# Kernel optimization log

Hardware: AMD Instinct MI355X
Metric: run time of the kernel (lower is better)

Reference implementation:

```python
import jax, jax.numpy as jnp
import numpy as np

B, S, T = 4, 1024, 2048
HID = 1024
NH = 16
NKV = 4
HD = HID // NH  # 64


def setup_inputs() -> dict:
    key = jax.random.key(0)
    ks = jax.random.split(key, 6)
    scale = 1.0 / np.sqrt(HID)
    return {
        "x": jax.random.normal(ks[0], (B, S, HID), dtype=jnp.float32),
        "context": jax.random.normal(ks[1], (B, T, HID), dtype=jnp.float32),
        "Wq": jax.random.normal(ks[2], (NH * HD, HID), dtype=jnp.float32) * scale,
        "Wk": jax.random.normal(ks[3], (NKV * HD, HID), dtype=jnp.float32) * scale,
        "Wv": jax.random.normal(ks[4], (NKV * HD, HID), dtype=jnp.float32) * scale,
        "Wo": jax.random.normal(ks[5], (HID, NH * HD), dtype=jnp.float32) * scale,
    }


def reference(x, context, Wq, Wk, Wv, Wo):
    Bx, Sx, _ = x.shape
    Tx = context.shape[1]
    rep = NH // NKV
    # projections (Linear with no bias: y = x @ W.T)
    q = (x @ Wq.T).reshape(Bx, Sx, NKV, rep, HD)          # group query heads by KV head
    k = (context @ Wk.T).reshape(Bx, Tx, NKV, HD)
    v = (context @ Wv.T).reshape(Bx, Tx, NKV, HD)
    scale = 1.0 / jnp.sqrt(jnp.asarray(HD, dtype=q.dtype))
    # scores: [B, NKV, rep, S, T] -- shares K across the rep grouped heads
    # (math-identical to repeat_interleave then SDPA, without materializing K/V copies)
    scores = jnp.einsum("bsgrd,btgd->bgrst", q, k) * scale
    attn = jax.nn.softmax(scores, axis=-1)
    out = jnp.einsum("bgrst,btgd->bsgrd", attn, v)        # [B,S,NKV,rep,HD]
    out = out.reshape(Bx, Sx, NH * HD)
    return out @ Wo.T
```

## Files before the change

### kernel.cpp

```cpp
#include <hip/hip_runtime.h>
#include <hip/hip_bf16.h>
#include <stdint.h>

typedef __bf16 bf16x8 __attribute__((ext_vector_type(8)));
typedef float f32x4 __attribute__((ext_vector_type(4)));
typedef unsigned short u16;
typedef unsigned int u32;

struct __align__(8) us4 { u16 x, y, z, w; };
struct __align__(16) us8 { u16 v[8]; };

#define LOG2E 1.44269504088896f
#define QSCALE (0.125f * LOG2E)

__device__ __forceinline__ void async_load16(const void* g, void* l) {
    __builtin_amdgcn_global_load_lds(
        (const __attribute__((address_space(1))) u32*)(uintptr_t)g,
        (__attribute__((address_space(3))) u32*)(u32)(uintptr_t)l,
        16, 0, 0);
}

__device__ __forceinline__ u16 f2bfbits(float f) {
    __bf16 h = (__bf16)f;
    return __builtin_bit_cast(u16, h);
}

__global__ __launch_bounds__(256) void convert_all(
    const float* __restrict__ x, const float* __restrict__ ctx,
    const float* __restrict__ wq, const float* __restrict__ wk,
    const float* __restrict__ wv, const float* __restrict__ wo,
    u16* __restrict__ xb, u16* __restrict__ ctxb, u16* __restrict__ wqb,
    u16* __restrict__ wkb, u16* __restrict__ wvb, u16* __restrict__ wob) {
    int i = blockIdx.x * 256 + threadIdx.x;
    const float* s; u16* d; int j;
    if (i < 524288)        { s = x;   d = xb;   j = i; }
    else if (i < 1572864)  { s = ctx; d = ctxb; j = i - 524288; }
    else if (i < 1703936)  { s = wq;  d = wqb;  j = i - 1572864; }
    else if (i < 1736704)  { s = wk;  d = wkb;  j = i - 1703936; }
    else if (i < 1769472)  { s = wv;  d = wvb;  j = i - 1736704; }
    else                   { s = wo;  d = wob;  j = i - 1769472; }
    const float4* sp = (const float4*)s + (size_t)j * 2;
    float4 a = sp[0], b = sp[1];
    us8 o;
    o.v[0] = f2bfbits(a.x); o.v[1] = f2bfbits(a.y);
    o.v[2] = f2bfbits(a.z); o.v[3] = f2bfbits(a.w);
    o.v[4] = f2bfbits(b.x); o.v[5] = f2bfbits(b.y);
    o.v[6] = f2bfbits(b.z); o.v[7] = f2bfbits(b.w);
    *(us8*)(d + (size_t)j * 8) = o;
}

__global__ __launch_bounds__(256) void proj_qkv(
    const u16* __restrict__ xb, const u16* __restrict__ ctxb,
    const u16* __restrict__ Wqb, const u16* __restrict__ Wkb,
    const u16* __restrict__ Wvb,
    u16* __restrict__ q, u16* __restrict__ k2, u16* __restrict__ vT) {
    __shared__ u16 As[128 * 64];
    __shared__ u16 Bs[128 * 64];
    const int tid = threadIdx.x;
    const int w = tid >> 6, lane = tid & 63, quad = lane >> 4, id = lane & 15;
    const int wr = (w >> 1) * 64, wc = (w & 1) * 64;
    const int lrow = lane >> 3, lcol = (lane & 7) * 8;

    const int bid = blockIdx.x;
    const u16 *A, *Bm;
    int mtile, ntile, mode;
    if (bid < 256) {
        mode = 0; A = xb; Bm = Wqb;
        mtile = (bid >> 3) * 128; ntile = (bid & 7) * 128;
    } else if (bid < 384) {
        int s2 = bid - 256;
        mode = 1; A = ctxb; Bm = Wkb;
        mtile = (s2 >> 1) * 128; ntile = (s2 & 1) * 128;
    } else {
        int s2 = bid - 384;
        mode = 2; A = ctxb; Bm = Wvb;
        mtile = (s2 >> 1) * 128; ntile = (s2 & 1) * 128;
    }

    f32x4 acc[4][4];
#pragma unroll
    for (int i = 0; i < 4; i++)
#pragma unroll
        for (int j = 0; j < 4; j++) acc[i][j] = (f32x4){0.f, 0.f, 0.f, 0.f};

    for (int k0 = 0; k0 < 1024; k0 += 64) {
        __syncthreads();
#pragma unroll
        for (int is = 0; is < 4; is++) {
            int r = is * 32 + w * 8 + lrow;
            async_load16(A + (size_t)(mtile + r) * 1024 + k0 + lcol, &As[(is * 32 + w * 8) * 64]);
        }
#pragma unroll
        for (int is = 0; is < 4; is++) {
            int r = is * 32 + w * 8 + lrow;
            async_load16(Bm + (size_t)(ntile + r) * 1024 + k0 + lcol, &Bs[(is * 32 + w * 8) * 64]);
        }
        __syncthreads();
#pragma unroll
        for (int kk = 0; kk < 2; kk++) {
            bf16x8 af[4], bfr[4];
#pragma unroll
            for (int i = 0; i < 4; i++)
                af[i] = *(const bf16x8*)&As[(wr + i * 16 + id) * 64 + kk * 32 + quad * 8];
#pragma unroll
            for (int j = 0; j < 4; j++)
                bfr[j] = *(const bf16x8*)&Bs[(wc + j * 16 + id) * 64 + kk * 32 + quad * 8];
#pragma unroll
            for (int i = 0; i < 4; i++)
#pragma unroll
                for (int j = 0; j < 4; j++)
                    acc[i][j] = __builtin_amdgcn_mfma_f32_16x16x32_bf16(af[i], bfr[j], acc[i][j], 0, 0, 0);
        }
    }

#pragma unroll
    for (int i = 0; i < 4; i++)
#pragma unroll
        for (int j = 0; j < 4; j++) {
            int mbase = mtile + wr + i * 16 + quad * 4;
            int n = ntile + wc + j * 16 + id;
            if (mode == 2) {
                int b = mbase >> 11, t = mbase & 2047;
                int g = n >> 6, d = n & 63;
                us4 pk;
                pk.x = f2bfbits(acc[i][j][0]);
                pk.y = f2bfbits(acc[i][j][1]);
                pk.z = f2bfbits(acc[i][j][2]);
                pk.w = f2bfbits(acc[i][j][3]);
                *(us4*)&vT[((size_t)((b << 2) + g) * 64 + d) * 2048 + t] = pk;
            } else if (mode == 1) {
#pragma unroll
                for (int r = 0; r < 4; r++) {
                    int m = mbase + r;
                    int b = m >> 11, t = m & 2047;
                    int g = n >> 6, d = n & 63;
                    k2[((size_t)((b << 2) + g) * 2048 + t) * 64 + d] = f2bfbits(acc[i][j][r]);
                }
            } else {
#pragma unroll
                for (int r = 0; r < 4; r++)
                    q[(size_t)(mbase + r) * 1024 + n] = f2bfbits(acc[i][j][r] * QSCALE);
            }
        }
}

__global__ __launch_bounds__(256) void gemm_out(const u16* __restrict__ A,
                                                const u16* __restrict__ Bm,
                                                float* __restrict__ C) {
    __shared__ u16 As[128 * 64];
    __shared__ u16 Bs[128 * 64];
    const int tid = threadIdx.x;
    const int w = tid >> 6, lane = tid & 63, quad = lane >> 4, id = lane & 15;
    const int mtile = blockIdx.y * 128, ntile = blockIdx.x * 128;
    const int wr = (w >> 1) * 64, wc = (w & 1) * 64;
    const int lrow = lane >> 3, lcol = (lane & 7) * 8;

    f32x4 acc[4][4];
#pragma unroll
    for (int i = 0; i < 4; i++)
#pragma unroll
        for (int j = 0; j < 4; j++) acc[i][j] = (f32x4){0.f, 0.f, 0.f, 0.f};

    for (int k0 = 0; k0 < 1024; k0 += 64) {
        __syncthreads();
#pragma unroll
        for (int is = 0; is < 4; is++) {
            int r = is * 32 + w * 8 + lrow;
            async_load16(A + (size_t)(mtile + r) * 1024 + k0 + lcol, &As[(is * 32 + w * 8) * 64]);
        }
#pragma unroll
        for (int is = 0; is < 4; is++) {
            int r = is * 32 + w * 8 + lrow;
            async_load16(Bm + (size_t)(ntile + r) * 1024 + k0 + lcol, &Bs[(is * 32 + w * 8) * 64]);
        }
        __syncthreads();
#pragma unroll
        for (int kk = 0; kk < 2; kk++) {
            bf16x8 af[4], bfr[4];
#pragma unroll
            for (int i = 0; i < 4; i++)
                af[i] = *(const bf16x8*)&As[(wr + i * 16 + id) * 64 + kk * 32 + quad * 8];
#pragma unroll
            for (int j = 0; j < 4; j++)
                bfr[j] = *(const bf16x8*)&Bs[(wc + j * 16 + id) * 64 + kk * 32 + quad * 8];
#pragma unroll
            for (int i = 0; i < 4; i++)
#pragma unroll
                for (int j = 0; j < 4; j++)
                    acc[i][j] = __builtin_amdgcn_mfma_f32_16x16x32_bf16(af[i], bfr[j], acc[i][j], 0, 0, 0);
        }
    }

#pragma unroll
    for (int i = 0; i < 4; i++)
#pragma unroll
        for (int j = 0; j < 4; j++) {
            int mbase = mtile + wr + i * 16 + quad * 4;
            int n = ntile + wc + j * 16 + id;
#pragma unroll
            for (int r = 0; r < 4; r++)
                C[(size_t)(mbase + r) * 1024 + n] = acc[i][j][r];
        }
}

__global__ __launch_bounds__(256, 2) void attn_kernel(const u16* __restrict__ q,
                                                      const u16* __restrict__ k2,
                                                      const u16* __restrict__ vT,
                                                      u16* __restrict__ o) {
    __shared__ u16 Ks[2][64 * 64];
    __shared__ u16 Vt[2][64 * 64];
    const int tid = threadIdx.x;
    const int w = tid >> 6, lane = tid & 63, quad = lane >> 4, id = lane & 15;

    const int bid = blockIdx.x;
    const int xcd = bid & 7, slot = bid >> 3;
    const int bg = xcd * 2 + (slot >> 5);
    const int inner = slot & 31;
    const int b = bg >> 2, g = bg & 3;
    const int h = g * 4 + (inner >> 3);
    const int s0 = (inner & 7) * 128;

    const int stgswz = (((lane & 7) ^ (lane >> 3) ^ ((w & 1) << 2))) * 8;
    int kfkey[2];
#pragma unroll
    for (int c = 0; c < 2; c++)
        kfkey[c] = (id & 3) | (((c ^ ((id >> 2) & 1)) & 1) << 2);
    const int vkey = (id & 7) ^ (((id >> 3) & 1) << 2);
    const int trow_base = ((id & 12) << 1) + (id & 3);

    bf16x8 qf[2][2];
#pragma unroll
    for (int rb = 0; rb < 2; rb++) {
        const size_t base = ((size_t)(b * 1024 + s0 + w * 32 + rb * 16 + id)) * 1024 + h * 64;
        qf[rb][0] = *(const bf16x8*)&q[base + quad * 8];
        qf[rb][1] = *(const bf16x8*)&q[base + 32 + quad * 8];
    }

    bf16x8 ones;
    {
        __bf16 one = (__bf16)1.0f;
#pragma unroll
        for (int i = 0; i < 8; i++) ones[i] = one;
    }

    f32x4 acc[2][4], accl[2];
#pragma unroll
    for (int rb = 0; rb < 2; rb++) {
        accl[rb] = (f32x4){0.f, 0.f, 0.f, 0.f};
#pragma unroll
        for (int i = 0; i < 4; i++) acc[rb][i] = (f32x4){0.f, 0.f, 0.f, 0.f};
    }

    const size_t kbase = ((size_t)(b * 4 + g)) * 2048 * 64;
    const size_t vbase = ((size_t)(b * 4 + g)) * 64 * 2048;

    auto stage = [&](int t0, int buf) {
#pragma unroll
        for (int is = 0; is < 2; is++) {
            int tl = is * 32 + w * 8;
            async_load16(&k2[kbase + (size_t)(t0 + tl + (lane >> 3)) * 64 + stgswz],
                         &Ks[buf][tl * 64]);
        }
#pragma unroll
        for (int is = 0; is < 2; is++) {
            int dl = is * 32 + w * 8;
            async_load16(&vT[vbase + (size_t)(dl + (lane >> 3)) * 2048 + t0 + stgswz],
                         &Vt[buf][dl * 64]);
        }
    };

    stage(0, 0);
    __syncthreads();

    int cur = 0;
    for (int t0 = 0; t0 < 2048; t0 += 64) {
        if (t0 + 64 < 2048) stage(t0 + 64, cur ^ 1);

        f32x4 s[2][2][2];
#pragma unroll
        for (int kk = 0; kk < 2; kk++)
#pragma unroll
            for (int P = 0; P < 2; P++)
#pragma unroll
                for (int c = 0; c < 2; c++) {
                    int trow = P * 32 + trow_base + c * 4;
                    bf16x8 kf = *(const bf16x8*)&Ks[cur][trow * 64 + (((kk * 4 + quad) ^ kfkey[c]) * 8)];
#pragma unroll
                    for (int rb = 0; rb < 2; rb++)
                        s[rb][P][c] = __builtin_amdgcn_mfma_f32_16x16x32_bf16(
                            kf, qf[rb][kk],
                            kk ? s[rb][P][c] : (f32x4){0.f, 0.f, 0.f, 0.f}, 0, 0, 0);
                }

        bf16x8 pa[2][2];
#pragma unroll
        for (int rb = 0; rb < 2; rb++)
#pragma unroll
            for (int P = 0; P < 2; P++) {
                bf16x8 t;
#pragma unroll
                for (int c = 0; c < 2; c++)
#pragma unroll
                    for (int r = 0; r < 4; r++)
                        t[c * 4 + r] = (__bf16)__builtin_exp2f(s[rb][P][c][r]);
                pa[rb][P] = t;
            }

#pragma unroll
        for (int P = 0; P < 2; P++) {
#pragma unroll
            for (int db = 0; db < 4; db++) {
                bf16x8 vf = *(const bf16x8*)&Vt[cur][(db * 16 + id) * 64 + (((P * 4 + quad) ^ vkey) * 8)];
#pragma unroll
                for (int rb = 0; rb < 2; rb++)
                    acc[rb][db] = __builtin_amdgcn_mfma_f32_16x16x32_bf16(pa[rb][P], vf, acc[rb][db], 0, 0, 0);
            }
#pragma unroll
            for (int rb = 0; rb < 2; rb++)
                accl[rb] = __builtin_amdgcn_mfma_f32_16x16x32_bf16(pa[rb][P], ones, accl[rb], 0, 0, 0);
        }

        __syncthreads();
        cur ^= 1;
    }

#pragma unroll
    for (int rb = 0; rb < 2; rb++) {
        f32x4 inv;
#pragma unroll
        for (int r = 0; r < 4; r++) inv[r] = 1.0f / accl[rb][r];
#pragma unroll
        for (int db = 0; db < 4; db++)
#pragma unroll
            for (int r = 0; r < 4; r++) {
                int srow = s0 + w * 32 + rb * 16 + quad * 4 + r;
                o[((size_t)(b * 1024 + srow)) * 1024 + h * 64 + db * 16 + id] =
                    f2bfbits(acc[rb][db][r] * inv[r]);
            }
    }
}

extern "C" void kernel_launch(void* const* d_in, const int* in_sizes, int n_in,
                              void* d_out, int out_size, void* d_ws, size_t ws_size,
                              hipStream_t stream) {
    (void)in_sizes; (void)n_in; (void)out_size; (void)ws_size;
    const float* x   = (const float*)d_in[0];
    const float* ctx = (const float*)d_in[1];
    const float* Wq  = (const float*)d_in[2];
    const float* Wk  = (const float*)d_in[3];
    const float* Wv  = (const float*)d_in[4];
    const float* Wo  = (const float*)d_in[5];
    float* out = (float*)d_out;

    u16* xb   = (u16*)d_ws;
    u16* ctxb = xb   + 4096 * 1024;
    u16* Wqb  = ctxb + 4 * 2048 * 1024;
    u16* Wkb  = Wqb  + 1024 * 1024;
    u16* Wvb  = Wkb  + 256 * 1024;
    u16* Wob  = Wvb  + 256 * 1024;
    u16* q    = Wob  + 1024 * 1024;
    u16* k2   = q    + 4096 * 1024;
    u16* vT   = k2   + 4 * 4 * 2048 * 64;
    u16* o    = vT   + 4 * 4 * 64 * 2048;

    convert_all<<<7424, 256, 0, stream>>>(x, ctx, Wq, Wk, Wv, Wo,
                                          xb, ctxb, Wqb, Wkb, Wvb, Wob);
    proj_qkv<<<512, 256, 0, stream>>>(xb, ctxb, Wqb, Wkb, Wvb, q, k2, vT);
    attn_kernel<<<512, 256, 0, stream>>>(q, k2, vT, o);
    gemm_out<<<dim3(8, 32), 256, 0, stream>>>(o, Wob, out);
}
```

Before: 210.4 us.

## Fuse fp32-to-bf16 conversion into GEMM loads and use fp16 for PV

Removes the separate conversion kernel. The projection and output GEMMs now stage fp32 tiles into LDS with an XOR swizzle and convert them to bf16 when building fragments. This saves one pass over the inputs and one launch, but doubles LDS use and global-to-LDS traffic per tile in the GEMMs. Separately, V and the softmax probabilities switch to fp16 with packed RTZ conversion and fp16 MFMA for the PV product, which cuts conversion instruction cost and changes precision behaviour. The output GEMM's A tile also gets a swizzled layout to reduce bank conflicts.

```diff
diff --git a/kernel.cpp b/kernel.cpp
--- a/kernel.cpp
+++ b/kernel.cpp
@@ -3,12 +3,13 @@
 #include <stdint.h>
 
 typedef __bf16 bf16x8 __attribute__((ext_vector_type(8)));
+typedef _Float16 f16x8 __attribute__((ext_vector_type(8)));
+typedef _Float16 f16x2 __attribute__((ext_vector_type(2)));
 typedef float f32x4 __attribute__((ext_vector_type(4)));
 typedef unsigned short u16;
 typedef unsigned int u32;
 
 struct __align__(8) us4 { u16 x, y, z, w; };
-struct __align__(16) us8 { u16 v[8]; };
 
 #define LOG2E 1.44269504088896f
 #define QSCALE (0.125f * LOG2E)
@@ -24,56 +25,49 @@
     __bf16 h = (__bf16)f;
     return __builtin_bit_cast(u16, h);
 }
-
-__global__ __launch_bounds__(256) void convert_all(
+__device__ __forceinline__ u16 f2hbits(float f) {
+    _Float16 h = (_Float16)f;
+    return __builtin_bit_cast(u16, h);
+}
+__device__ __forceinline__ f16x2 pkrtz(float a, float b) {
+    return __builtin_bit_cast(f16x2, __builtin_amdgcn_cvt_pkrtz(a, b));
+}
+
+__device__ __forceinline__ bf16x8 frag_from_f32(const float* T, int row, int kkq2, int id) {
+    const float4 lo = *(const float4*)&T[row * 64 + (((kkq2) ^ id) << 2)];
+    const float4 hi = *(const float4*)&T[row * 64 + (((kkq2 + 1) ^ id) << 2)];
+    bf16x8 f;
+    f[0] = (__bf16)lo.x; f[1] = (__bf16)lo.y; f[2] = (__bf16)lo.z; f[3] = (__bf16)lo.w;
+    f[4] = (__bf16)hi.x; f[5] = (__bf16)hi.y; f[6] = (__bf16)hi.z; f[7] = (__bf16)hi.w;
+    return f;
+}
+
+__global__ __launch_bounds__(256) void proj_qkv(
     const float* __restrict__ x, const float* __restrict__ ctx,
-    const float* __restrict__ wq, const float* __restrict__ wk,
-    const float* __restrict__ wv, const float* __restrict__ wo,
-    u16* __restrict__ xb, u16* __restrict__ ctxb, u16* __restrict__ wqb,
-    u16* __restrict__ wkb, u16* __restrict__ wvb, u16* __restrict__ wob) {
-    int i = blockIdx.x * 256 + threadIdx.x;
-    const float* s; u16* d; int j;
-    if (i < 524288)        { s = x;   d = xb;   j = i; }
-    else if (i < 1572864)  { s = ctx; d = ctxb; j = i - 524288; }
-    else if (i < 1703936)  { s = wq;  d = wqb;  j = i - 1572864; }
-    else if (i < 1736704)  { s = wk;  d = wkb;  j = i - 1703936; }
-    else if (i < 1769472)  { s = wv;  d = wvb;  j = i - 1736704; }
-    else                   { s = wo;  d = wob;  j = i - 1769472; }
-    const float4* sp = (const float4*)s + (size_t)j * 2;
-    float4 a = sp[0], b = sp[1];
-    us8 o;
-    o.v[0] = f2bfbits(a.x); o.v[1] = f2bfbits(a.y);
-    o.v[2] = f2bfbits(a.z); o.v[3] = f2bfbits(a.w);
-    o.v[4] = f2bfbits(b.x); o.v[5] = f2bfbits(b.y);
-    o.v[6] = f2bfbits(b.z); o.v[7] = f2bfbits(b.w);
-    *(us8*)(d + (size_t)j * 8) = o;
-}
-
-__global__ __launch_bounds__(256) void proj_qkv(
-    const u16* __restrict__ xb, const u16* __restrict__ ctxb,
-    const u16* __restrict__ Wqb, const u16* __restrict__ Wkb,
-    const u16* __restrict__ Wvb,
+    const float* __restrict__ Wq, const float* __restrict__ Wk,
+    const float* __restrict__ Wv,
     u16* __restrict__ q, u16* __restrict__ k2, u16* __restrict__ vT) {
-    __shared__ u16 As[128 * 64];
-    __shared__ u16 Bs[128 * 64];
+    __shared__ float As[128 * 64];
+    __shared__ float Bs[128 * 64];
     const int tid = threadIdx.x;
     const int w = tid >> 6, lane = tid & 63, quad = lane >> 4, id = lane & 15;
     const int wr = (w >> 1) * 64, wc = (w & 1) * 64;
-    const int lrow = lane >> 3, lcol = (lane & 7) * 8;
+    const int arow = lane >> 4;
+    const int swzcb = (lane & 15) ^ (w * 4 + arow);
 
     const int bid = blockIdx.x;
-    const u16 *A, *Bm;
+    const float *A, *Bm;
     int mtile, ntile, mode;
     if (bid < 256) {
-        mode = 0; A = xb; Bm = Wqb;
+        mode = 0; A = x; Bm = Wq;
         mtile = (bid >> 3) * 128; ntile = (bid & 7) * 128;
     } else if (bid < 384) {
         int s2 = bid - 256;
-        mode = 1; A = ctxb; Bm = Wkb;
+        mode = 1; A = ctx; Bm = Wk;
         mtile = (s2 >> 1) * 128; ntile = (s2 & 1) * 128;
     } else {
         int s2 = bid - 384;
-        mode = 2; A = ctxb; Bm = Wvb;
+        mode = 2; A = ctx; Bm = Wv;
         mtile = (s2 >> 1) * 128; ntile = (s2 & 1) * 128;
     }
 
@@ -86,25 +80,28 @@
     for (int k0 = 0; k0 < 1024; k0 += 64) {
         __syncthreads();
 #pragma unroll
-        for (int is = 0; is < 4; is++) {
-            int r = is * 32 + w * 8 + lrow;
-            async_load16(A + (size_t)(mtile + r) * 1024 + k0 + lcol, &As[(is * 32 + w * 8) * 64]);
-        }
-#pragma unroll
-        for (int is = 0; is < 4; is++) {
-            int r = is * 32 + w * 8 + lrow;
-            async_load16(Bm + (size_t)(ntile + r) * 1024 + k0 + lcol, &Bs[(is * 32 + w * 8) * 64]);
+        for (int is = 0; is < 8; is++) {
+            int base = is * 16 + w * 4;
+            async_load16(A + (size_t)(mtile + base + arow) * 1024 + k0 + swzcb * 4,
+                         &As[base * 64]);
+        }
+#pragma unroll
+        for (int is = 0; is < 8; is++) {
+            int base = is * 16 + w * 4;
+            async_load16(Bm + (size_t)(ntile + base + arow) * 1024 + k0 + swzcb * 4,
+                         &Bs[base * 64]);
         }
         __syncthreads();
 #pragma unroll
         for (int kk = 0; kk < 2; kk++) {
+            const int kkq2 = kk * 8 + quad * 2;
             bf16x8 af[4], bfr[4];
 #pragma unroll
             for (int i = 0; i < 4; i++)
-                af[i] = *(const bf16x8*)&As[(wr + i * 16 + id) * 64 + kk * 32 + quad * 8];
+                af[i] = frag_from_f32(As, wr + i * 16 + id, kkq2, id);
 #pragma unroll
             for (int j = 0; j < 4; j++)
-                bfr[j] = *(const bf16x8*)&Bs[(wc + j * 16 + id) * 64 + kk * 32 + quad * 8];
+                bfr[j] = frag_from_f32(Bs, wc + j * 16 + id, kkq2, id);
 #pragma unroll
             for (int i = 0; i < 4; i++)
 #pragma unroll
@@ -123,10 +120,10 @@
                 int b = mbase >> 11, t = mbase & 2047;
                 int g = n >> 6, d = n & 63;
                 us4 pk;
-                pk.x = f2bfbits(acc[i][j][0]);
-                pk.y = f2bfbits(acc[i][j][1]);
-                pk.z = f2bfbits(acc[i][j][2]);
-                pk.w = f2bfbits(acc[i][j][3]);
+                pk.x = f2hbits(acc[i][j][0]);
+                pk.y = f2hbits(acc[i][j][1]);
+                pk.z = f2hbits(acc[i][j][2]);
+                pk.w = f2hbits(acc[i][j][3]);
                 *(us4*)&vT[((size_t)((b << 2) + g) * 64 + d) * 2048 + t] = pk;
             } else if (mode == 1) {
 #pragma unroll
@@ -145,15 +142,17 @@
 }
 
 __global__ __launch_bounds__(256) void gemm_out(const u16* __restrict__ A,
-                                                const u16* __restrict__ Bm,
+                                                const float* __restrict__ Bm,
                                                 float* __restrict__ C) {
     __shared__ u16 As[128 * 64];
-    __shared__ u16 Bs[128 * 64];
+    __shared__ float Bs[128 * 64];
     const int tid = threadIdx.x;
     const int w = tid >> 6, lane = tid & 63, quad = lane >> 4, id = lane & 15;
     const int mtile = blockIdx.y * 128, ntile = blockIdx.x * 128;
     const int wr = (w >> 1) * 64, wc = (w & 1) * 64;
-    const int lrow = lane >> 3, lcol = (lane & 7) * 8;
+    const int arow = lane >> 4;
+    const int swzcb = (lane & 15) ^ (w * 4 + arow);
+    const int stgswz8 = ((lane & 7) ^ (lane >> 3)) * 8;
 
     f32x4 acc[4][4];
 #pragma unroll
@@ -165,24 +164,29 @@
         __syncthreads();
 #pragma unroll
         for (int is = 0; is < 4; is++) {
-            int r = is * 32 + w * 8 + lrow;
-            async_load16(A + (size_t)(mtile + r) * 1024 + k0 + lcol, &As[(is * 32 + w * 8) * 64]);
-        }
-#pragma unroll
-        for (int is = 0; is < 4; is++) {
-            int r = is * 32 + w * 8 + lrow;
-            async_load16(Bm + (size_t)(ntile + r) * 1024 + k0 + lcol, &Bs[(is * 32 + w * 8) * 64]);
+            int base = is * 32 + w * 8;
+            async_load16(A + (size_t)(mtile + base + (lane >> 3)) * 1024 + k0 + stgswz8,
+                         &As[base * 64]);
+        }
+#pragma unroll
+        for (int is = 0; is < 8; is++) {
+            int base = is * 16 + w * 4;
+            async_load16(Bm + (size_t)(ntile + base + arow) * 1024 + k0 + swzcb * 4,
+                         &Bs[base * 64]);
         }
         __syncthreads();
 #pragma unroll
         for (int kk = 0; kk < 2; kk++) {
+            const int kkq2 = kk * 8 + quad * 2;
             bf16x8 af[4], bfr[4];
 #pragma unroll
-            for (int i = 0; i < 4; i++)
-                af[i] = *(const bf16x8*)&As[(wr + i * 16 + id) * 64 + kk * 32 + quad * 8];
+            for (int i = 0; i < 4; i++) {
+                int row = wr + i * 16 + id;
+                af[i] = *(const bf16x8*)&As[row * 64 + (((kk * 4 + quad) ^ (id & 7)) * 8)];
+            }
 #pragma unroll
             for (int j = 0; j < 4; j++)
-                bfr[j] = *(const bf16x8*)&Bs[(wc + j * 16 + id) * 64 + kk * 32 + quad * 8];
+                bfr[j] = frag_from_f32(Bs, wc + j * 16 + id, kkq2, id);
 #pragma unroll
             for (int i = 0; i < 4; i++)
 #pragma unroll
@@ -236,12 +240,9 @@
         qf[rb][1] = *(const bf16x8*)&q[base + 32 + quad * 8];
     }
 
-    bf16x8 ones;
-    {
-        __bf16 one = (__bf16)1.0f;
-#pragma unroll
-        for (int i = 0; i < 8; i++) ones[i] = one;
-    }
+    f16x8 ones;
+#pragma unroll
+    for (int i = 0; i < 8; i++) ones[i] = (_Float16)1.0f;
 
     f32x4 acc[2][4], accl[2];
 #pragma unroll
@@ -292,32 +293,37 @@
                             kk ? s[rb][P][c] : (f32x4){0.f, 0.f, 0.f, 0.f}, 0, 0, 0);
                 }
 
-        bf16x8 pa[2][2];
+        f16x8 pa[2][2];
+        union PU { f16x8 v; f16x2 h[4]; };
 #pragma unroll
         for (int rb = 0; rb < 2; rb++)
 #pragma unroll
             for (int P = 0; P < 2; P++) {
-                bf16x8 t;
-#pragma unroll
-                for (int c = 0; c < 2; c++)
-#pragma unroll
-                    for (int r = 0; r < 4; r++)
-                        t[c * 4 + r] = (__bf16)__builtin_exp2f(s[rb][P][c][r]);
-                pa[rb][P] = t;
+                PU u;
+#pragma unroll
+                for (int c = 0; c < 2; c++) {
+                    float e0 = __builtin_exp2f(s[rb][P][c][0]);
+                    float e1 = __builtin_exp2f(s[rb][P][c][1]);
+                    float e2 = __builtin_exp2f(s[rb][P][c][2]);
+                    float e3 = __builtin_exp2f(s[rb][P][c][3]);
+                    u.h[c * 2 + 0] = pkrtz(e0, e1);
+                    u.h[c * 2 + 1] = pkrtz(e2, e3);
+                }
+                pa[rb][P] = u.v;
             }
 
 #pragma unroll
         for (int P = 0; P < 2; P++) {
 #pragma unroll
             for (int db = 0; db < 4; db++) {
-                bf16x8 vf = *(const bf16x8*)&Vt[cur][(db * 16 + id) * 64 + (((P * 4 + quad) ^ vkey) * 8)];
+                f16x8 vf = *(const f16x8*)&Vt[cur][(db * 16 + id) * 64 + (((P * 4 + quad) ^ vkey) * 8)];
 #pragma unroll
                 for (int rb = 0; rb < 2; rb++)
-                    acc[rb][db] = __builtin_amdgcn_mfma_f32_16x16x32_bf16(pa[rb][P], vf, acc[rb][db], 0, 0, 0);
+                    acc[rb][db] = __builtin_amdgcn_mfma_f32_16x16x32_f16(pa[rb][P], vf, acc[rb][db], 0, 0, 0);
             }
 #pragma unroll
             for (int rb = 0; rb < 2; rb++)
-                accl[rb] = __builtin_amdgcn_mfma_f32_16x16x32_bf16(pa[rb][P], ones, accl[rb], 0, 0, 0);
+                accl[rb] = __builtin_amdgcn_mfma_f32_16x16x32_f16(pa[rb][P], ones, accl[rb], 0, 0, 0);
         }
 
         __syncthreads();
@@ -352,20 +358,12 @@
     const float* Wo  = (const float*)d_in[5];
     float* out = (float*)d_out;
 
-    u16* xb   = (u16*)d_ws;
-    u16* ctxb = xb   + 4096 * 1024;
-    u16* Wqb  = ctxb + 4 * 2048 * 1024;
-    u16* Wkb  = Wqb  + 1024 * 1024;
-    u16* Wvb  = Wkb  + 256 * 1024;
-    u16* Wob  = Wvb  + 256 * 1024;
-    u16* q    = Wob  + 1024 * 1024;
-    u16* k2   = q    + 4096 * 1024;
-    u16* vT   = k2   + 4 * 4 * 2048 * 64;
-    u16* o    = vT   + 4 * 4 * 64 * 2048;
-
-    convert_all<<<7424, 256, 0, stream>>>(x, ctx, Wq, Wk, Wv, Wo,
-                                          xb, ctxb, Wqb, Wkb, Wvb, Wob);
-    proj_qkv<<<512, 256, 0, stream>>>(xb, ctxb, Wqb, Wkb, Wvb, q, k2, vT);
+    u16* q  = (u16*)d_ws;
+    u16* k2 = q + 4096 * 1024;
+    u16* vT = k2 + 4 * 4 * 2048 * 64;
+    u16* o  = vT + 4 * 4 * 64 * 2048;
+
+    proj_qkv<<<512, 256, 0, stream>>>(x, ctx, Wq, Wk, Wv, q, k2, vT);
     attn_kernel<<<512, 256, 0, stream>>>(q, k2, vT, o);
-    gemm_out<<<dim3(8, 32), 256, 0, stream>>>(o, Wob, out);
-}
+    gemm_out<<<dim3(8, 32), 256, 0, stream>>>(o, Wo, out);
+}
```

Result: slower. 215.1 us (+2.2%).
